# Performance work log

Measured on AMD Instinct MI355X. Metric: run time of the kernel, lower is better.

Reference implementation:

```python
import jax, jax.numpy as jnp
import numpy as np
from jax import lax

# dims
B, N, F = 128, 65536, 512


def setup_inputs() -> dict:
    key = jax.random.key(0)
    k1, k2 = jax.random.split(key)
    x = jax.random.normal(k1, (B, N), dtype=jnp.float32)          # dry audio
    logits = jax.random.normal(k2, (B, F, 5), dtype=jnp.float32)  # [bs, n_frames, 5]
    return {"x": x, "logits": logits}


def linear_interpolate_dim1(v, n_out):
    # v: [B, n_in, C] -> [B, n_out, C], linear interp with align_corners=True
    n_in = v.shape[1]
    pos = jnp.arange(n_out, dtype=jnp.float32) * ((n_in - 1) / (n_out - 1))
    i0 = jnp.clip(jnp.floor(pos).astype(jnp.int32), 0, n_in - 2)
    frac = (pos - i0.astype(jnp.float32))[None, :, None]
    return v[:, i0, :] * (1.0 - frac) + v[:, i0 + 1, :] * frac


def logits_to_a_coeff_triangle(a_logits):
    # stability-triangle parameterization: |a2| < 1 and |a1| < 1 + a2
    a1 = 2.0 * jnp.tanh(a_logits[..., 0])
    a1_abs = jnp.abs(a1)
    a2 = 0.5 * ((2.0 - a1_abs) * jnp.tanh(a_logits[..., 1]) + a1_abs)
    return jnp.stack([a1, a2], axis=-1)  # [B, F, 2]


def sample_wise_lpc2(x, a):
    # y[n] = x[n] - a1[n]*y[n-1] - a2[n]*y[n-2];  x: [B,N], a: [B,N,2]
    def step(carry, inp):
        y1, y2 = carry
        xn, a1, a2 = inp
        y = xn - a1 * y1 - a2 * y2
        return (y, y1), y
    z = jnp.zeros(x.shape[0], dtype=x.dtype)
    xs = (x.T, a[:, :, 0].T, a[:, :, 1].T)  # time-major
    _, ys = lax.scan(step, (z, z), xs)
    return ys.T


def time_varying_fir(x, b):
    # y[n] = b0[n]*x[n] + b1[n]*x[n-1] + b2[n]*x[n-2];  b: [B,N,3]
    xp = jnp.pad(x, ((0, 0), (2, 0)))
    return b[:, :, 0] * xp[:, 2:] + b[:, :, 1] * xp[:, 1:-1] + b[:, :, 2] * xp[:, :-2]


def reference(x, logits):
    n_samples = x.shape[1]
    # interp_logits=False: map a-logits to coeffs at frame rate, then interpolate
    a_coeff = logits_to_a_coeff_triangle(logits[..., :2])          # [B, F, 2]
    b_coeff = logits[..., 2:]                                      # [B, F, 3]
    a_coeff = linear_interpolate_dim1(a_coeff, n_samples)          # [B, N, 2]
    b_coeff = linear_interpolate_dim1(b_coeff, n_samples)          # [B, N, 3]
    y_a = sample_wise_lpc2(x, a_coeff)
    y_ab = time_varying_fir(y_a, b_coeff)
    return y_ab
```

## Files before the change

kernel.cpp:

```cpp
#include <hip/hip_runtime.h>
#include <hip/hip_bf16.h>

#define B_   128
#define N_   65536
#define F_   512
#define CS   64
#define CPR  (N_ / CS)
#define TPB  128
#define CPB  TPB
#define BPR  (CPR / CPB)
#define NBLK (B_ * BPR)
#define BLK_SAMP (TPB * CS)
#define KPOS ((float)(511.0 / 65535.0))
#define STRIDE 68

#define OFF_AGG   0
#define OFF_START (NBLK * 6)

__device__ __forceinline__ void load_acoef(const float* Lg, int i, float& a1, float& a2) {
    float l0 = Lg[i * 5 + 0], l1 = Lg[i * 5 + 1];
    a1 = 2.0f * tanhf(l0);
    float ab = fabsf(a1);
    a2 = 0.5f * ((2.0f - ab) * tanhf(l1) + ab);
}

__global__ __launch_bounds__(TPB) void phaseA(const float* __restrict__ x,
                                              const float* __restrict__ logits,
                                              float* __restrict__ blockAgg) {
    __shared__ __align__(16) float buf[TPB][STRIDE];
    __shared__ float sc[6][TPB];
    int tid = threadIdx.x;
    int gchunk0 = blockIdx.x * TPB;

    const float4* xg = (const float4*)x + (size_t)gchunk0 * (CS / 4);
    #pragma unroll
    for (int it = 0; it < BLK_SAMP / 4 / TPB; ++it) {
        int i4 = it * TPB + tid;
        float4 v = xg[i4];
        *(float4*)&buf[i4 >> 4][(i4 & 15) * 4] = v;
    }
    __syncthreads();

    int t = gchunk0 + tid;
    int b = t >> 10;
    int c = t & (CPR - 1);
    int n0 = c * CS;

    int I  = min((int)floorf((float)n0 * KPOS), F_ - 2);
    int I2 = min(I + 2, F_ - 1);
    const float* Lg = logits + (size_t)b * F_ * 5;
    float a1A, a2A, a1B, a2B, a1C, a2C;
    load_acoef(Lg, I,     a1A, a2A);
    load_acoef(Lg, I + 1, a1B, a2B);
    load_acoef(Lg, I2,    a1C, a2C);

    float A00 = 1.f, A01 = 0.f, A10 = 0.f, A11 = 1.f, v0 = 0.f, v1 = 0.f;
    #pragma unroll 4
    for (int j = 0; j < CS / 4; ++j) {
        float4 xv = *(const float4*)&buf[tid][j * 4];
        #pragma unroll
        for (int u = 0; u < 4; ++u) {
            int k = j * 4 + u;
            float xn = (&xv.x)[u];
            float pos = (float)(n0 + k) * KPOS;
            int i0 = min((int)floorf(pos), F_ - 2);
            float frac = pos - (float)i0;
            float om = 1.0f - frac;
            bool sel = i0 > I;
            float a1 = om * (sel ? a1B : a1A) + frac * (sel ? a1C : a1B);
            float a2 = om * (sel ? a2B : a2A) + frac * (sel ? a2C : a2B);
            float nA00 = -a1 * A00 - a2 * A10;
            float nA01 = -a1 * A01 - a2 * A11;
            float nv0  = xn - a1 * v0 - a2 * v1;
            A10 = A00; A11 = A01; v1 = v0;
            A00 = nA00; A01 = nA01; v0 = nv0;
        }
    }

    for (int d = 1; d < TPB; d <<= 1) {
        sc[0][tid] = A00; sc[1][tid] = A01; sc[2][tid] = A10;
        sc[3][tid] = A11; sc[4][tid] = v0;  sc[5][tid] = v1;
        __syncthreads();
        if (tid >= d) {
            float f00 = sc[0][tid - d], f01 = sc[1][tid - d];
            float f10 = sc[2][tid - d], f11 = sc[3][tid - d];
            float fv0 = sc[4][tid - d], fv1 = sc[5][tid - d];
            float n00 = A00 * f00 + A01 * f10;
            float n01 = A00 * f01 + A01 * f11;
            float n10 = A10 * f00 + A11 * f10;
            float n11 = A10 * f01 + A11 * f11;
            float nv0 = A00 * fv0 + A01 * fv1 + v0;
            float nv1 = A10 * fv0 + A11 * fv1 + v1;
            A00 = n00; A01 = n01; A10 = n10; A11 = n11; v0 = nv0; v1 = nv1;
        }
        __syncthreads();
    }
    if (tid == TPB - 1) {
        float* T = blockAgg + (size_t)blockIdx.x * 6;
        T[0] = A00; T[1] = A01; T[2] = A10; T[3] = A11; T[4] = v0; T[5] = v1;
    }
}

__global__ __launch_bounds__(TPB) void phaseB(const float* __restrict__ blockAgg,
                                              float* __restrict__ blockStart) {
    int r = threadIdx.x;
    float s0 = 0.f, s1 = 0.f;
    #pragma unroll
    for (int j = 0; j < BPR; ++j) {
        int g = r * BPR + j;
        blockStart[g * 2 + 0] = s0;
        blockStart[g * 2 + 1] = s1;
        const float* T = blockAgg + (size_t)g * 6;
        float n0 = T[0] * s0 + T[1] * s1 + T[4];
        float n1 = T[2] * s0 + T[3] * s1 + T[5];
        s0 = n0; s1 = n1;
    }
}

__global__ __launch_bounds__(TPB) void phaseC(const float* __restrict__ x,
                                              const float* __restrict__ logits,
                                              const float* __restrict__ blockStart,
                                              float* __restrict__ out) {
    __shared__ __align__(16) float buf[TPB][STRIDE];
    __shared__ float sc[6][TPB];
    int tid = threadIdx.x;
    int gchunk0 = blockIdx.x * TPB;

    const float4* xg = (const float4*)x + (size_t)gchunk0 * (CS / 4);
    #pragma unroll
    for (int it = 0; it < BLK_SAMP / 4 / TPB; ++it) {
        int i4 = it * TPB + tid;
        float4 v = xg[i4];
        *(float4*)&buf[i4 >> 4][(i4 & 15) * 4] = v;
    }
    __syncthreads();

    int t = gchunk0 + tid;
    int b = t >> 10;
    int c = t & (CPR - 1);
    int n0 = c * CS;

    int I  = min((int)floorf((float)n0 * KPOS), F_ - 2);
    int I2 = min(I + 2, F_ - 1);
    const float* Lg = logits + (size_t)b * F_ * 5;
    float cA[5], cB[5], cC[5];
    load_acoef(Lg, I,     cA[0], cA[1]);
    load_acoef(Lg, I + 1, cB[0], cB[1]);
    load_acoef(Lg, I2,    cC[0], cC[1]);
    #pragma unroll
    for (int j = 0; j < 3; ++j) {
        cA[2 + j] = Lg[I * 5 + 2 + j];
        cB[2 + j] = Lg[(I + 1) * 5 + 2 + j];
        cC[2 + j] = Lg[I2 * 5 + 2 + j];
    }

    float A00 = 1.f, A01 = 0.f, A10 = 0.f, A11 = 1.f, v0 = 0.f, v1 = 0.f;
    #pragma unroll 4
    for (int j = 0; j < CS / 4; ++j) {
        float4 xv = *(const float4*)&buf[tid][j * 4];
        #pragma unroll
        for (int u = 0; u < 4; ++u) {
            int k = j * 4 + u;
            float xn = (&xv.x)[u];
            float pos = (float)(n0 + k) * KPOS;
            int i0 = min((int)floorf(pos), F_ - 2);
            float frac = pos - (float)i0;
            float om = 1.0f - frac;
            bool sel = i0 > I;
            float a1 = om * (sel ? cB[0] : cA[0]) + frac * (sel ? cC[0] : cB[0]);
            float a2 = om * (sel ? cB[1] : cA[1]) + frac * (sel ? cC[1] : cB[1]);
            float nA00 = -a1 * A00 - a2 * A10;
            float nA01 = -a1 * A01 - a2 * A11;
            float nv0  = xn - a1 * v0 - a2 * v1;
            A10 = A00; A11 = A01; v1 = v0;
            A00 = nA00; A01 = nA01; v0 = nv0;
        }
    }

    for (int d = 1; d < TPB; d <<= 1) {
        sc[0][tid] = A00; sc[1][tid] = A01; sc[2][tid] = A10;
        sc[3][tid] = A11; sc[4][tid] = v0;  sc[5][tid] = v1;
        __syncthreads();
        if (tid >= d) {
            float f00 = sc[0][tid - d], f01 = sc[1][tid - d];
            float f10 = sc[2][tid - d], f11 = sc[3][tid - d];
            float fv0 = sc[4][tid - d], fv1 = sc[5][tid - d];
            float n00 = A00 * f00 + A01 * f10;
            float n01 = A00 * f01 + A01 * f11;
            float n10 = A10 * f00 + A11 * f10;
            float n11 = A10 * f01 + A11 * f11;
            float nv0 = A00 * fv0 + A01 * fv1 + v0;
            float nv1 = A10 * fv0 + A11 * fv1 + v1;
            A00 = n00; A01 = n01; A10 = n10; A11 = n11; v0 = nv0; v1 = nv1;
        }
        __syncthreads();
    }
    sc[0][tid] = A00; sc[1][tid] = A01; sc[2][tid] = A10;
    sc[3][tid] = A11; sc[4][tid] = v0;  sc[5][tid] = v1;
    __syncthreads();

    float bs0 = blockStart[(size_t)blockIdx.x * 2 + 0];
    float bs1 = blockStart[(size_t)blockIdx.x * 2 + 1];
    float s0v, s1v;
    if (tid == 0) {
        s0v = bs0; s1v = bs1;
    } else {
        float L00 = sc[0][tid - 1], L01 = sc[1][tid - 1];
        float L10 = sc[2][tid - 1], L11 = sc[3][tid - 1];
        float Lv0 = sc[4][tid - 1], Lv1 = sc[5][tid - 1];
        s0v = L00 * bs0 + L01 * bs1 + Lv0;
        s1v = L10 * bs0 + L11 * bs1 + Lv1;
    }
    __syncthreads();

    #pragma unroll 4
    for (int j = 0; j < CS / 4; ++j) {
        float4 xv = *(const float4*)&buf[tid][j * 4];
        float4 yv;
        #pragma unroll
        for (int u = 0; u < 4; ++u) {
            int k = j * 4 + u;
            float xn = (&xv.x)[u];
            float pos = (float)(n0 + k) * KPOS;
            int i0 = min((int)floorf(pos), F_ - 2);
            float frac = pos - (float)i0;
            float om = 1.0f - frac;
            bool sel = i0 > I;
            float a1 = om * (sel ? cB[0] : cA[0]) + frac * (sel ? cC[0] : cB[0]);
            float a2 = om * (sel ? cB[1] : cA[1]) + frac * (sel ? cC[1] : cB[1]);
            float b0 = om * (sel ? cB[2] : cA[2]) + frac * (sel ? cC[2] : cB[2]);
            float b1 = om * (sel ? cB[3] : cA[3]) + frac * (sel ? cC[3] : cB[3]);
            float b2 = om * (sel ? cB[4] : cA[4]) + frac * (sel ? cC[4] : cB[4]);
            float y = xn - a1 * s0v - a2 * s1v;
            (&yv.x)[u] = b0 * y + b1 * s0v + b2 * s1v;
            s1v = s0v; s0v = y;
        }
        *(float4*)&buf[tid][j * 4] = yv;
    }
    __syncthreads();

    float4* og = (float4*)out + (size_t)gchunk0 * (CS / 4);
    #pragma unroll
    for (int it = 0; it < BLK_SAMP / 4 / TPB; ++it) {
        int i4 = it * TPB + tid;
        og[i4] = *(float4*)&buf[i4 >> 4][(i4 & 15) * 4];
    }
}

extern "C" void kernel_launch(void* const* d_in, const int* in_sizes, int n_in,
                              void* d_out, int out_size, void* d_ws, size_t ws_size,
                              hipStream_t stream) {
    const float* x      = (const float*)d_in[0];
    const float* logits = (const float*)d_in[1];
    float* out = (float*)d_out;
    float* ws  = (float*)d_ws;

    float* blockAgg   = ws + OFF_AGG;
    float* blockStart = ws + OFF_START;

    phaseA<<<NBLK, TPB, 0, stream>>>(x, logits, blockAgg);
    phaseB<<<1, TPB, 0, stream>>>(blockAgg, blockStart);
    phaseC<<<NBLK, TPB, 0, stream>>>(x, logits, blockStart, out);
}
```

Before: 109.8 us.

## Store per-chunk scan prefixes, drop phaseB, and linearize coefficient interpolation

phaseA now writes each thread's exclusive intra-block prefix transform to the workspace, so phaseC no longer re-runs the chunk recurrence and block scan. The separate single-block phaseB is removed, and each phaseC block folds the preceding block aggregates of its row serially in thread 0. Per-sample interpolation is replaced by precomputed affine coefficients with a split point kc, cutting floor/convert work in the inner loops. The cost is extra global traffic for six prefix floats per chunk and a serial loop of up to seven steps in phaseC's thread 0.

Result: faster. 101.0 us (-8.1%).

```diff
diff --git a/kernel.cpp b/kernel.cpp
--- a/kernel.cpp
+++ b/kernel.cpp
@@ -7,30 +7,42 @@
 #define CS   64
 #define CPR  (N_ / CS)
 #define TPB  128
-#define CPB  TPB
-#define BPR  (CPR / CPB)
+#define BPR  (CPR / TPB)
 #define NBLK (B_ * BPR)
 #define BLK_SAMP (TPB * CS)
+#define NT   (B_ * CPR)
 #define KPOS ((float)(511.0 / 65535.0))
+#define INVK ((float)(65535.0 / 511.0))
 #define STRIDE 68
 
-#define OFF_AGG   0
-#define OFF_START (NBLK * 6)
-
-__device__ __forceinline__ void load_acoef(const float* Lg, int i, float& a1, float& a2) {
-    float l0 = Lg[i * 5 + 0], l1 = Lg[i * 5 + 1];
-    a1 = 2.0f * tanhf(l0);
-    float ab = fabsf(a1);
-    a2 = 0.5f * ((2.0f - ab) * tanhf(l1) + ab);
-}
-
-__global__ __launch_bounds__(TPB) void phaseA(const float* __restrict__ x,
-                                              const float* __restrict__ logits,
-                                              float* __restrict__ blockAgg) {
+#define OFF_PREF 0
+#define OFF_AGG  (6 * NT)
+
+__device__ __forceinline__ float tanh_map1(float l) { return 2.0f * tanhf(l); }
+
+__device__ __forceinline__ void chunk_geom(int n0, float& pos0, int& I, int& kc) {
+    pos0 = (float)n0 * KPOS;
+    I = min((int)pos0, F_ - 2);
+    int k = (int)ceilf(((float)(I + 1) - pos0) * INVK);
+    k = max(0, min(k, CS));
+    if (k > 0 && (int)((float)(n0 + k - 1) * KPOS) > I) --k;
+    else if (k < CS && (int)((float)(n0 + k) * KPOS) <= I) ++k;
+    if ((int)pos0 > F_ - 2) k = CS;
+    if (I == F_ - 2) {
+        if ((float)n0 * KPOS >= (float)(F_ - 1)) k = CS;
+    }
+    kc = k;
+}
+
+__global__ __launch_bounds__(TPB, 2) void phaseA(const float* __restrict__ x,
+                                                 const float* __restrict__ logits,
+                                                 float* __restrict__ pref,
+                                                 float* __restrict__ agg) {
     __shared__ __align__(16) float buf[TPB][STRIDE];
     __shared__ float sc[6][TPB];
     int tid = threadIdx.x;
-    int gchunk0 = blockIdx.x * TPB;
+    int gid = blockIdx.x;
+    int gchunk0 = gid * TPB;
 
     const float4* xg = (const float4*)x + (size_t)gchunk0 * (CS / 4);
     #pragma unroll
@@ -46,32 +58,41 @@
     int c = t & (CPR - 1);
     int n0 = c * CS;
 
-    int I  = min((int)floorf((float)n0 * KPOS), F_ - 2);
+    float pos0; int I, kc;
+    chunk_geom(n0, pos0, I, kc);
     int I2 = min(I + 2, F_ - 1);
     const float* Lg = logits + (size_t)b * F_ * 5;
-    float a1A, a2A, a1B, a2B, a1C, a2C;
-    load_acoef(Lg, I,     a1A, a2A);
-    load_acoef(Lg, I + 1, a1B, a2B);
-    load_acoef(Lg, I2,    a1C, a2C);
+    float a1A = tanh_map1(Lg[I * 5 + 0]);
+    float a1B = tanh_map1(Lg[(I + 1) * 5 + 0]);
+    float a1C = tanh_map1(Lg[I2 * 5 + 0]);
+    float t1A = tanhf(Lg[I * 5 + 1]);
+    float t1B = tanhf(Lg[(I + 1) * 5 + 1]);
+    float t1C = tanhf(Lg[I2 * 5 + 1]);
+    float a2A = 0.5f * ((2.0f - fabsf(a1A)) * t1A + fabsf(a1A));
+    float a2B = 0.5f * ((2.0f - fabsf(a1B)) * t1B + fabsf(a1B));
+    float a2C = 0.5f * ((2.0f - fabsf(a1C)) * t1C + fabsf(a1C));
+
+    float If = (float)I;
+    float C1  = fmaf(pos0 - If,        a1B - a1A, a1A), D1  = KPOS * (a1B - a1A);
+    float C1b = fmaf(pos0 - If - 1.f,  a1C - a1B, a1B), D1b = KPOS * (a1C - a1B);
+    float C2  = fmaf(pos0 - If,        a2B - a2A, a2A), D2  = KPOS * (a2B - a2A);
+    float C2b = fmaf(pos0 - If - 1.f,  a2C - a2B, a2B), D2b = KPOS * (a2C - a2B);
 
     float A00 = 1.f, A01 = 0.f, A10 = 0.f, A11 = 1.f, v0 = 0.f, v1 = 0.f;
-    #pragma unroll 4
+    #pragma unroll
     for (int j = 0; j < CS / 4; ++j) {
         float4 xv = *(const float4*)&buf[tid][j * 4];
         #pragma unroll
         for (int u = 0; u < 4; ++u) {
             int k = j * 4 + u;
             float xn = (&xv.x)[u];
-            float pos = (float)(n0 + k) * KPOS;
-            int i0 = min((int)floorf(pos), F_ - 2);
-            float frac = pos - (float)i0;
-            float om = 1.0f - frac;
-            bool sel = i0 > I;
-            float a1 = om * (sel ? a1B : a1A) + frac * (sel ? a1C : a1B);
-            float a2 = om * (sel ? a2B : a2A) + frac * (sel ? a2C : a2B);
-            float nA00 = -a1 * A00 - a2 * A10;
-            float nA01 = -a1 * A01 - a2 * A11;
-            float nv0  = xn - a1 * v0 - a2 * v1;
+            bool sB = (k >= kc);
+            float kf = (float)k;
+            float a1 = fmaf(kf, sB ? D1b : D1, sB ? C1b : C1);
+            float a2 = fmaf(kf, sB ? D2b : D2, sB ? C2b : C2);
+            float nA00 = fmaf(-a2, A10, -a1 * A00);
+            float nA01 = fmaf(-a2, A11, -a1 * A01);
+            float nv0  = fmaf(-a2, v1, fmaf(-a1, v0, xn));
             A10 = A00; A11 = A01; v1 = v0;
             A00 = nA00; A01 = nA01; v0 = nv0;
         }
@@ -95,36 +116,36 @@
         }
         __syncthreads();
     }
+    sc[0][tid] = A00; sc[1][tid] = A01; sc[2][tid] = A10;
+    sc[3][tid] = A11; sc[4][tid] = v0;  sc[5][tid] = v1;
+    __syncthreads();
+
+    float e00, e01, e10, e11, ev0, ev1;
+    if (tid == 0) { e00 = 1.f; e01 = 0.f; e10 = 0.f; e11 = 1.f; ev0 = 0.f; ev1 = 0.f; }
+    else {
+        e00 = sc[0][tid - 1]; e01 = sc[1][tid - 1];
+        e10 = sc[2][tid - 1]; e11 = sc[3][tid - 1];
+        ev0 = sc[4][tid - 1]; ev1 = sc[5][tid - 1];
+    }
+    pref[0 * NT + t] = e00; pref[1 * NT + t] = e01;
+    pref[2 * NT + t] = e10; pref[3 * NT + t] = e11;
+    pref[4 * NT + t] = ev0; pref[5 * NT + t] = ev1;
     if (tid == TPB - 1) {
-        float* T = blockAgg + (size_t)blockIdx.x * 6;
+        float* T = agg + (size_t)gid * 6;
         T[0] = A00; T[1] = A01; T[2] = A10; T[3] = A11; T[4] = v0; T[5] = v1;
     }
 }
 
-__global__ __launch_bounds__(TPB) void phaseB(const float* __restrict__ blockAgg,
-                                              float* __restrict__ blockStart) {
-    int r = threadIdx.x;
-    float s0 = 0.f, s1 = 0.f;
-    #pragma unroll
-    for (int j = 0; j < BPR; ++j) {
-        int g = r * BPR + j;
-        blockStart[g * 2 + 0] = s0;
-        blockStart[g * 2 + 1] = s1;
-        const float* T = blockAgg + (size_t)g * 6;
-        float n0 = T[0] * s0 + T[1] * s1 + T[4];
-        float n1 = T[2] * s0 + T[3] * s1 + T[5];
-        s0 = n0; s1 = n1;
-    }
-}
-
-__global__ __launch_bounds__(TPB) void phaseC(const float* __restrict__ x,
-                                              const float* __restrict__ logits,
-                                              const float* __restrict__ blockStart,
-                                              float* __restrict__ out) {
+__global__ __launch_bounds__(TPB, 2) void phaseC(const float* __restrict__ x,
+                                                 const float* __restrict__ logits,
+                                                 const float* __restrict__ pref,
+                                                 const float* __restrict__ agg,
+                                                 float* __restrict__ out) {
     __shared__ __align__(16) float buf[TPB][STRIDE];
-    __shared__ float sc[6][TPB];
+    __shared__ float sbs[2];
     int tid = threadIdx.x;
-    int gchunk0 = blockIdx.x * TPB;
+    int gid = blockIdx.x;
+    int gchunk0 = gid * TPB;
 
     const float4* xg = (const float4*)x + (size_t)gchunk0 * (CS / 4);
     #pragma unroll
@@ -133,87 +154,68 @@
         float4 v = xg[i4];
         *(float4*)&buf[i4 >> 4][(i4 & 15) * 4] = v;
     }
-    __syncthreads();
+
+    if (tid == 0) {
+        float s0 = 0.f, s1 = 0.f;
+        int p0 = gid & ~(BPR - 1);
+        for (int p = p0; p < gid; ++p) {
+            const float* T = agg + (size_t)p * 6;
+            float n0s = T[0] * s0 + T[1] * s1 + T[4];
+            float n1s = T[2] * s0 + T[3] * s1 + T[5];
+            s0 = n0s; s1 = n1s;
+        }
+        sbs[0] = s0; sbs[1] = s1;
+    }
 
     int t = gchunk0 + tid;
     int b = t >> 10;
     int c = t & (CPR - 1);
     int n0 = c * CS;
 
-    int I  = min((int)floorf((float)n0 * KPOS), F_ - 2);
+    float pos0; int I, kc;
+    chunk_geom(n0, pos0, I, kc);
     int I2 = min(I + 2, F_ - 1);
     const float* Lg = logits + (size_t)b * F_ * 5;
-    float cA[5], cB[5], cC[5];
-    load_acoef(Lg, I,     cA[0], cA[1]);
-    load_acoef(Lg, I + 1, cB[0], cB[1]);
-    load_acoef(Lg, I2,    cC[0], cC[1]);
-    #pragma unroll
-    for (int j = 0; j < 3; ++j) {
-        cA[2 + j] = Lg[I * 5 + 2 + j];
-        cB[2 + j] = Lg[(I + 1) * 5 + 2 + j];
-        cC[2 + j] = Lg[I2 * 5 + 2 + j];
-    }
-
-    float A00 = 1.f, A01 = 0.f, A10 = 0.f, A11 = 1.f, v0 = 0.f, v1 = 0.f;
-    #pragma unroll 4
-    for (int j = 0; j < CS / 4; ++j) {
-        float4 xv = *(const float4*)&buf[tid][j * 4];
+    float vA[5], vB[5], vC[5];
+    {
+        float a1A = tanh_map1(Lg[I * 5 + 0]);
+        float a1B = tanh_map1(Lg[(I + 1) * 5 + 0]);
+        float a1C = tanh_map1(Lg[I2 * 5 + 0]);
+        float t1A = tanhf(Lg[I * 5 + 1]);
+        float t1B = tanhf(Lg[(I + 1) * 5 + 1]);
+        float t1C = tanhf(Lg[I2 * 5 + 1]);
+        vA[0] = a1A; vB[0] = a1B; vC[0] = a1C;
+        vA[1] = 0.5f * ((2.0f - fabsf(a1A)) * t1A + fabsf(a1A));
+        vB[1] = 0.5f * ((2.0f - fabsf(a1B)) * t1B + fabsf(a1B));
+        vC[1] = 0.5f * ((2.0f - fabsf(a1C)) * t1C + fabsf(a1C));
         #pragma unroll
-        for (int u = 0; u < 4; ++u) {
-            int k = j * 4 + u;
-            float xn = (&xv.x)[u];
-            float pos = (float)(n0 + k) * KPOS;
-            int i0 = min((int)floorf(pos), F_ - 2);
-            float frac = pos - (float)i0;
-            float om = 1.0f - frac;
-            bool sel = i0 > I;
-            float a1 = om * (sel ? cB[0] : cA[0]) + frac * (sel ? cC[0] : cB[0]);
-            float a2 = om * (sel ? cB[1] : cA[1]) + frac * (sel ? cC[1] : cB[1]);
-            float nA00 = -a1 * A00 - a2 * A10;
-            float nA01 = -a1 * A01 - a2 * A11;
-            float nv0  = xn - a1 * v0 - a2 * v1;
-            A10 = A00; A11 = A01; v1 = v0;
-            A00 = nA00; A01 = nA01; v0 = nv0;
-        }
-    }
-
-    for (int d = 1; d < TPB; d <<= 1) {
-        sc[0][tid] = A00; sc[1][tid] = A01; sc[2][tid] = A10;
-        sc[3][tid] = A11; sc[4][tid] = v0;  sc[5][tid] = v1;
-        __syncthreads();
-        if (tid >= d) {
-            float f00 = sc[0][tid - d], f01 = sc[1][tid - d];
-            float f10 = sc[2][tid - d], f11 = sc[3][tid - d];
-            float fv0 = sc[4][tid - d], fv1 = sc[5][tid - d];
-            float n00 = A00 * f00 + A01 * f10;
-            float n01 = A00 * f01 + A01 * f11;
-            float n10 = A10 * f00 + A11 * f10;
-            float n11 = A10 * f01 + A11 * f11;
-            float nv0 = A00 * fv0 + A01 * fv1 + v0;
-            float nv1 = A10 * fv0 + A11 * fv1 + v1;
-            A00 = n00; A01 = n01; A10 = n10; A11 = n11; v0 = nv0; v1 = nv1;
-        }
-        __syncthreads();
-    }
-    sc[0][tid] = A00; sc[1][tid] = A01; sc[2][tid] = A10;
-    sc[3][tid] = A11; sc[4][tid] = v0;  sc[5][tid] = v1;
-    __syncthreads();
-
-    float bs0 = blockStart[(size_t)blockIdx.x * 2 + 0];
-    float bs1 = blockStart[(size_t)blockIdx.x * 2 + 1];
-    float s0v, s1v;
-    if (tid == 0) {
-        s0v = bs0; s1v = bs1;
-    } else {
-        float L00 = sc[0][tid - 1], L01 = sc[1][tid - 1];
-        float L10 = sc[2][tid - 1], L11 = sc[3][tid - 1];
-        float Lv0 = sc[4][tid - 1], Lv1 = sc[5][tid - 1];
-        s0v = L00 * bs0 + L01 * bs1 + Lv0;
-        s1v = L10 * bs0 + L11 * bs1 + Lv1;
-    }
-    __syncthreads();
-
-    #pragma unroll 4
+        for (int j = 0; j < 3; ++j) {
+            vA[2 + j] = Lg[I * 5 + 2 + j];
+            vB[2 + j] = Lg[(I + 1) * 5 + 2 + j];
+            vC[2 + j] = Lg[I2 * 5 + 2 + j];
+        }
+    }
+    float If = (float)I;
+    float Cs[5], Ds[5], Csb[5], Dsb[5];
+    #pragma unroll
+    for (int j = 0; j < 5; ++j) {
+        Cs[j]  = fmaf(pos0 - If,       vB[j] - vA[j], vA[j]);
+        Ds[j]  = KPOS * (vB[j] - vA[j]);
+        Csb[j] = fmaf(pos0 - If - 1.f, vC[j] - vB[j], vB[j]);
+        Dsb[j] = KPOS * (vC[j] - vB[j]);
+    }
+
+    float L00 = pref[0 * NT + t], L01 = pref[1 * NT + t];
+    float L10 = pref[2 * NT + t], L11 = pref[3 * NT + t];
+    float Lv0 = pref[4 * NT + t], Lv1 = pref[5 * NT + t];
+
+    __syncthreads();
+
+    float bs0 = sbs[0], bs1 = sbs[1];
+    float s0v = L00 * bs0 + L01 * bs1 + Lv0;
+    float s1v = L10 * bs0 + L11 * bs1 + Lv1;
+
+    #pragma unroll
     for (int j = 0; j < CS / 4; ++j) {
         float4 xv = *(const float4*)&buf[tid][j * 4];
         float4 yv;
@@ -221,18 +223,15 @@
         for (int u = 0; u < 4; ++u) {
             int k = j * 4 + u;
             float xn = (&xv.x)[u];
-            float pos = (float)(n0 + k) * KPOS;
-            int i0 = min((int)floorf(pos), F_ - 2);
-            float frac = pos - (float)i0;
-            float om = 1.0f - frac;
-            bool sel = i0 > I;
-            float a1 = om * (sel ? cB[0] : cA[0]) + frac * (sel ? cC[0] : cB[0]);
-            float a2 = om * (sel ? cB[1] : cA[1]) + frac * (sel ? cC[1] : cB[1]);
-            float b0 = om * (sel ? cB[2] : cA[2]) + frac * (sel ? cC[2] : cB[2]);
-            float b1 = om * (sel ? cB[3] : cA[3]) + frac * (sel ? cC[3] : cB[3]);
-            float b2 = om * (sel ? cB[4] : cA[4]) + frac * (sel ? cC[4] : cB[4]);
-            float y = xn - a1 * s0v - a2 * s1v;
-            (&yv.x)[u] = b0 * y + b1 * s0v + b2 * s1v;
+            bool sB = (k >= kc);
+            float kf = (float)k;
+            float a1 = fmaf(kf, sB ? Dsb[0] : Ds[0], sB ? Csb[0] : Cs[0]);
+            float a2 = fmaf(kf, sB ? Dsb[1] : Ds[1], sB ? Csb[1] : Cs[1]);
+            float b0 = fmaf(kf, sB ? Dsb[2] : Ds[2], sB ? Csb[2] : Cs[2]);
+            float b1 = fmaf(kf, sB ? Dsb[3] : Ds[3], sB ? Csb[3] : Cs[3]);
+            float b2 = fmaf(kf, sB ? Dsb[4] : Ds[4], sB ? Csb[4] : Cs[4]);
+            float y = fmaf(-a2, s1v, fmaf(-a1, s0v, xn));
+            (&yv.x)[u] = fmaf(b2, s1v, fmaf(b1, s0v, b0 * y));
             s1v = s0v; s0v = y;
         }
         *(float4*)&buf[tid][j * 4] = yv;
@@ -255,10 +254,9 @@
     float* out = (float*)d_out;
     float* ws  = (float*)d_ws;
 
-    float* blockAgg   = ws + OFF_AGG;
-    float* blockStart = ws + OFF_START;
-
-    phaseA<<<NBLK, TPB, 0, stream>>>(x, logits, blockAgg);
-    phaseB<<<1, TPB, 0, stream>>>(blockAgg, blockStart);
-    phaseC<<<NBLK, TPB, 0, stream>>>(x, logits, blockStart, out);
-}
+    float* pref = ws + OFF_PREF;
+    float* agg  = ws + OFF_AGG;
+
+    phaseA<<<NBLK, TPB, 0, stream>>>(x, logits, pref, agg);
+    phaseC<<<NBLK, TPB, 0, stream>>>(x, logits, pref, agg, out);
+}
```
